# Kernel tuning notes

Hardware: AMD Instinct MI355X
Metric: run time of the kernel (lower is better)

The kernel has to match this reference:

```python
import jax, jax.numpy as jnp
import numpy as np

B, T, N_EMBED, HEAD = 512, 256, 384, 64
BLOCK = 256
SCALE = N_EMBED ** -0.5  # source scales by input-channel dim, not head_size


def setup_inputs() -> dict:
    key = jax.random.key(0)
    kx, kk, kq, kv = jax.random.split(key, 4)
    x = jax.random.normal(kx, (B, T, N_EMBED), dtype=jnp.float32)
    # torch Linear(n_embed, head_size, bias=False) weights, stored as (in, out)
    s = N_EMBED ** -0.5
    Wk = jax.random.normal(kk, (N_EMBED, HEAD), dtype=jnp.float32) * s
    Wq = jax.random.normal(kq, (N_EMBED, HEAD), dtype=jnp.float32) * s
    Wv = jax.random.normal(kv, (N_EMBED, HEAD), dtype=jnp.float32) * s
    return {"x": x, "Wk": Wk, "Wq": Wq, "Wv": Wv}


def reference(x, Wk, Wq, Wv):
    Bx, Tx, _ = x.shape
    K = jnp.einsum('btc,ch->bth', x, Wk)
    Q = jnp.einsum('btc,ch->bth', x, Wq)
    V = jnp.einsum('btc,ch->bth', x, Wv)
    scores = jnp.einsum('bth,bsh->bts', Q, K) * SCALE  # [B, T, T]
    causal = jnp.tril(jnp.ones((Tx, Tx), dtype=bool))
    scores = jnp.where(causal[None, :, :], scores, -jnp.inf)
    W = jax.nn.softmax(scores, axis=-1)
    # dropout is identity in eval mode (reference baseline is deterministic)
    out = jnp.einsum('bts,bsh->bth', W, V)
    return out
```

## Files before the change

kernel.cpp:

```cpp
#include <hip/hip_runtime.h>
#include <hip/hip_bf16.h>

#define B_  512
#define T_  256
#define C_  384
#define H_  64
#define SCALE_ 0.05103103630798287f

typedef float f32x4  __attribute__((ext_vector_type(4)));
typedef short bf16x8 __attribute__((ext_vector_type(8)));
typedef short bf16x4 __attribute__((ext_vector_type(4)));

__device__ __forceinline__ unsigned short f2bf(float f) {
    union { float f; unsigned u; } v; v.f = f;
    unsigned r = v.u + 0x7FFFu + ((v.u >> 16) & 1u);
    return (unsigned short)(r >> 16);
}
__device__ __forceinline__ unsigned cvt_pk_bf16(float lo, float hi) {
    unsigned r;
    asm("v_cvt_pk_bf16_f32 %0, %1, %2" : "=v"(r) : "v"(lo), "v"(hi));
    return r;
}
__device__ __forceinline__ int swz64(int row, int col) {
    return row * 64 + (((col >> 3) ^ (row & 7)) << 3) + (col & 7);
}

__global__ __launch_bounds__(1024, 4) void att_head_kernel(
    const float* __restrict__ x,  const float* __restrict__ Wk,
    const float* __restrict__ Wq, const float* __restrict__ Wv,
    float* __restrict__ out)
{
    __shared__ __align__(16) short smem[73728];
    short* const Ks = smem;
    short* const Vt = smem + 16384;
    short* const Pb = smem + 33280;

    const int tid  = threadIdx.x;
    const int b    = blockIdx.x;
    const int w    = tid >> 6;
    const int lane = tid & 63;
    const int g    = lane >> 4;
    const int i    = lane & 15;
    const int rb   = 16 * w;

    const float* xb = x + (size_t)b * T_ * C_;
    const float* Wm[3] = { Wk, Wq, Wv };

    f32x4 accP[12];
    #pragma unroll
    for (int nb = 0; nb < 12; nb++) accP[nb] = f32x4{0.f, 0.f, 0.f, 0.f};

    const float* xrow = xb + (size_t)(rb + i) * C_ + g * 8;

    {
        float wfa[12], wfb[12];
        auto loadWchunk = [&](int j, float* dst) {
            #pragma unroll
            for (int m = 0; m < 3; m++) {
                const float* Wp = Wm[m] + (size_t)(j * 64 + w * 4) * H_ + lane;
                #pragma unroll
                for (int jj = 0; jj < 4; jj++) dst[m * 4 + jj] = Wp[jj * H_];
            }
        };
        auto writeWchunk = [&](int j, const float* src) {
            short* buf = smem + j * 12288;
            #pragma unroll
            for (int m = 0; m < 3; m++) {
                union { unsigned u; short s[2]; } p0, p1;
                p0.u = cvt_pk_bf16(src[4 * m + 0], src[4 * m + 1]);
                p1.u = cvt_pk_bf16(src[4 * m + 2], src[4 * m + 3]);
                bf16x4 pk;
                pk[0] = p0.s[0]; pk[1] = p0.s[1]; pk[2] = p1.s[0]; pk[3] = p1.s[1];
                const int row = m * 64 + lane;
                const int k0  = w * 4;
                *(bf16x4*)&buf[row * 64 + (((k0 >> 3) ^ (row & 7)) << 3) + (k0 & 7)] = pk;
            }
        };
        loadWchunk(0, wfa);
        #pragma unroll
        for (int j = 0; j < 6; j++) {
            float* curW = (j & 1) ? wfb : wfa;
            float* nxtW = (j & 1) ? wfa : wfb;
            if (j < 5) loadWchunk(j + 1, nxtW);
            writeWchunk(j, curW);
        }
    }
    float4 xr[2][4];
    #pragma unroll
    for (int ks = 0; ks < 2; ks++)
        #pragma unroll
        for (int h = 0; h < 2; h++)
            xr[0][ks * 2 + h] = *(const float4*)(xrow + ks * 32 + h * 4);
    asm volatile("s_waitcnt lgkmcnt(0)\n\ts_barrier" ::: "memory");

    #pragma unroll
    for (int j = 0; j < 6; j++) {
        const int par = j & 1;
        const short* cur = smem + j * 12288;
        if (j < 5) {
            #pragma unroll
            for (int ks = 0; ks < 2; ks++)
                #pragma unroll
                for (int h = 0; h < 2; h++)
                    xr[par ^ 1][ks * 2 + h] = *(const float4*)(xrow + (j + 1) * 64 + ks * 32 + h * 4);
        }
        bf16x8 afs[2];
        #pragma unroll
        for (int ks = 0; ks < 2; ks++)
            #pragma unroll
            for (int h = 0; h < 2; h++) {
                const float4 v = xr[par][ks * 2 + h];
                afs[ks][h * 4 + 0] = (short)f2bf(v.x);
                afs[ks][h * 4 + 1] = (short)f2bf(v.y);
                afs[ks][h * 4 + 2] = (short)f2bf(v.z);
                afs[ks][h * 4 + 3] = (short)f2bf(v.w);
            }
        #pragma unroll
        for (int nb = 0; nb < 12; nb++) {
            #pragma unroll
            for (int ks = 0; ks < 2; ks++) {
                const int brow = nb * 16 + i;
                const bf16x8 bfr = *(const bf16x8*)&cur[brow * 64 + (((ks * 4 + g) ^ (i & 7)) << 3)];
                accP[nb] = __builtin_amdgcn_mfma_f32_16x16x32_bf16(afs[ks], bfr, accP[nb], 0, 0, 0);
            }
        }
    }
    asm volatile("s_waitcnt lgkmcnt(0)\n\ts_barrier" ::: "memory");

    #pragma unroll
    for (int nb = 0; nb < 4; nb++)
        #pragma unroll
        for (int r = 0; r < 4; r++)
            Ks[swz64(rb + 4 * g + r, 16 * nb + i)] = (short)f2bf(accP[4 + nb][r]);
    asm volatile("s_waitcnt lgkmcnt(0)" ::: "memory");
    bf16x8 qf[2];
    #pragma unroll
    for (int ks = 0; ks < 2; ks++)
        qf[ks] = *(const bf16x8*)&Ks[(rb + i) * 64 + (((4 * ks + g) ^ (i & 7)) << 3)];
    asm volatile("s_waitcnt lgkmcnt(0)" ::: "memory");
    #pragma unroll
    for (int nb = 0; nb < 4; nb++)
        #pragma unroll
        for (int r = 0; r < 4; r++)
            Ks[swz64(rb + 4 * g + r, 16 * nb + i)] = (short)f2bf(accP[nb][r]);
    #pragma unroll
    for (int nb = 0; nb < 4; nb++) {
        bf16x4 pk;
        #pragma unroll
        for (int r = 0; r < 4; r++) pk[r] = (short)f2bf(accP[8 + nb][r]);
        *(bf16x4*)&Vt[(16 * nb + i) * 264 + rb + 4 * g] = pk;
    }
    asm volatile("s_waitcnt lgkmcnt(0)\n\ts_barrier" ::: "memory");

    short* const myP = Pb + w * 1280;
    const float NEG_INF = -__builtin_inff();
    float mrun = NEG_INF, lrun = 0.f;
    f32x4 accO[4];
    #pragma unroll
    for (int ht = 0; ht < 4; ht++) accO[ht] = f32x4{0.f, 0.f, 0.f, 0.f};

    auto PVADD = [&](int bufsel, int ck) {
        const bf16x8 pf = *(const bf16x8*)&myP[bufsel * 640 + i * 40 + 8 * g];
        #pragma unroll
        for (int ht = 0; ht < 4; ht++) {
            const bf16x8 vf = *(const bf16x8*)&Vt[(16 * ht + i) * 264 + 32 * ck + 8 * g];
            accO[ht] = __builtin_amdgcn_mfma_f32_16x16x32_bf16(vf, pf, accO[ht], 0, 0, 0);
        }
    };

    const int npair = w >> 1;
    #pragma unroll
    for (int p = 0; p < 8; p++) {
        if (p <= npair) {
            f32x4 sA[2];
            sA[0] = f32x4{0.f, 0.f, 0.f, 0.f};
            sA[1] = f32x4{0.f, 0.f, 0.f, 0.f};
            #pragma unroll
            for (int s = 0; s < 2; s++) {
                const int nt = 2 * p + s;
                if (nt <= w) {
                    #pragma unroll
                    for (int ks = 0; ks < 2; ks++) {
                        const bf16x8 kfr = *(const bf16x8*)&Ks[(16 * nt + i) * 64 +
                                (((4 * ks + g) ^ (i & 7)) << 3)];
                        sA[s] = __builtin_amdgcn_mfma_f32_16x16x32_bf16(kfr, qf[ks], sA[s], 0, 0, 0);
                    }
                }
            }
            if (p > 0) PVADD((p - 1) & 1, p - 1);

            float mt = NEG_INF;
            #pragma unroll
            for (int s = 0; s < 2; s++)
                #pragma unroll
                for (int r = 0; r < 4; r++) {
                    const int kv = 16 * (2 * p + s) + 4 * g + r;
                    const bool ok = (2 * p + s <= w) && (kv <= rb + i);
                    const float v = ok ? sA[s][r] * SCALE_ : NEG_INF;
                    sA[s][r] = v;
                    mt = fmaxf(mt, v);
                }
            mt = fmaxf(mt, __shfl_xor(mt, 16, 64));
            mt = fmaxf(mt, __shfl_xor(mt, 32, 64));

            if (!__all(mt <= mrun + 8.0f)) {
                const float mnew = fmaxf(mrun, mt);
                const float f = __expf(mrun - mnew);
                mrun = mnew; lrun *= f;
                #pragma unroll
                for (int ht = 0; ht < 4; ht++)
                    #pragma unroll
                    for (int r = 0; r < 4; r++) accO[ht][r] *= f;
            }
            #pragma unroll
            for (int s = 0; s < 2; s++) {
                const float p0 = __expf(sA[s][0] - mrun);
                const float p1 = __expf(sA[s][1] - mrun);
                const float p2 = __expf(sA[s][2] - mrun);
                const float p3 = __expf(sA[s][3] - mrun);
                lrun += (p0 + p1) + (p2 + p3);
                union { bf16x4 v; unsigned u[2]; } pk;
                pk.u[0] = cvt_pk_bf16(p0, p1);
                pk.u[1] = cvt_pk_bf16(p2, p3);
                *(bf16x4*)&myP[(p & 1) * 640 + i * 40 + 16 * s + 4 * g] = pk.v;
            }
        }
    }
    PVADD(npair & 1, npair);

    lrun += __shfl_xor(lrun, 16, 64);
    lrun += __shfl_xor(lrun, 32, 64);
    const float inv = 1.f / lrun;

    float* orow = out + ((size_t)b * T_ + rb + i) * H_;
    #pragma unroll
    for (int ht = 0; ht < 4; ht++) {
        float4 o;
        o.x = accO[ht][0] * inv;
        o.y = accO[ht][1] * inv;
        o.z = accO[ht][2] * inv;
        o.w = accO[ht][3] * inv;
        *(float4*)&orow[16 * ht + 4 * g] = o;
    }
}

extern "C" void kernel_launch(void* const* d_in, const int* in_sizes, int n_in,
                              void* d_out, int out_size, void* d_ws, size_t ws_size,
                              hipStream_t stream) {
    const float* x  = (const float*)d_in[0];
    const float* Wk = (const float*)d_in[1];
    const float* Wq = (const float*)d_in[2];
    const float* Wv = (const float*)d_in[3];
    float* out = (float*)d_out;
    (void)d_ws; (void)ws_size; (void)in_sizes; (void)n_in; (void)out_size;
    att_head_kernel<<<dim3(B_), dim3(1024), 0, stream>>>(x, Wk, Wq, Wv, out);
}
```

Measured before the change: 56.89 us.

## Pre-transpose Wv to bf16 in workspace and read V weights from global

Adds a small pre-kernel that converts Wv to bf16 in a transposed layout inside the workspace. The main kernel then stages only Wk and Wq in shared memory and loads V-projection B fragments straight from global/L2. This shrinks LDS use per block and the per-block W staging work. The cost is an extra kernel launch and uncoalesced-ish global fragment loads inside the MFMA loop. The original kernel is kept as a fallback when no workspace is available.

```diff
diff --git a/kernel.cpp b/kernel.cpp
--- a/kernel.cpp
+++ b/kernel.cpp
@@ -25,12 +25,21 @@
     return row * 64 + (((col >> 3) ^ (row & 7)) << 3) + (col & 7);
 }
 
-__global__ __launch_bounds__(1024, 4) void att_head_kernel(
+__global__ void transpose_wv_kernel(const float* __restrict__ Wv, short* __restrict__ Wtv) {
+    const int idx = blockIdx.x * 256 + threadIdx.x;
+    const int n  = idx / 48;
+    const int kb = (idx % 48) * 8;
+    short* dst = Wtv + n * 384;
+    #pragma unroll
+    for (int k = kb; k < kb + 8; k++) dst[k] = (short)f2bf(Wv[(size_t)k * H_ + n]);
+}
+
+__global__ __launch_bounds__(1024, 4) void att_head_ws(
     const float* __restrict__ x,  const float* __restrict__ Wk,
-    const float* __restrict__ Wq, const float* __restrict__ Wv,
+    const float* __restrict__ Wq, const short* __restrict__ Wtv,
     float* __restrict__ out)
 {
-    __shared__ __align__(16) short smem[73728];
+    __shared__ __align__(16) short smem[53760];
     short* const Ks = smem;
     short* const Vt = smem + 16384;
     short* const Pb = smem + 33280;
@@ -44,7 +53,7 @@
     const int rb   = 16 * w;
 
     const float* xb = x + (size_t)b * T_ * C_;
-    const float* Wm[3] = { Wk, Wq, Wv };
+    const float* Wm[2] = { Wk, Wq };
 
     f32x4 accP[12];
     #pragma unroll
@@ -53,19 +62,19 @@
     const float* xrow = xb + (size_t)(rb + i) * C_ + g * 8;
 
     {
-        float wfa[12], wfb[12];
+        float wfa[8], wfb[8];
         auto loadWchunk = [&](int j, float* dst) {
             #pragma unroll
-            for (int m = 0; m < 3; m++) {
+            for (int m = 0; m < 2; m++) {
                 const float* Wp = Wm[m] + (size_t)(j * 64 + w * 4) * H_ + lane;
                 #pragma unroll
                 for (int jj = 0; jj < 4; jj++) dst[m * 4 + jj] = Wp[jj * H_];
             }
         };
         auto writeWchunk = [&](int j, const float* src) {
-            short* buf = smem + j * 12288;
-            #pragma unroll
-            for (int m = 0; m < 3; m++) {
+            short* buf = smem + j * 8192;
+            #pragma unroll
+            for (int m = 0; m < 2; m++) {
                 union { unsigned u; short s[2]; } p0, p1;
                 p0.u = cvt_pk_bf16(src[4 * m + 0], src[4 * m + 1]);
                 p1.u = cvt_pk_bf16(src[4 * m + 2], src[4 * m + 3]);
@@ -93,10 +102,11 @@
             xr[0][ks * 2 + h] = *(const float4*)(xrow + ks * 32 + h * 4);
     asm volatile("s_waitcnt lgkmcnt(0)\n\ts_barrier" ::: "memory");
 
+    const short* wtv0 = Wtv + (size_t)i * 384 + 8 * g;
     #pragma unroll
     for (int j = 0; j < 6; j++) {
         const int par = j & 1;
-        const short* cur = smem + j * 12288;
+        const short* cur = smem + j * 8192;
         if (j < 5) {
             #pragma unroll
             for (int ks = 0; ks < 2; ks++)
@@ -116,13 +126,20 @@
                 afs[ks][h * 4 + 3] = (short)f2bf(v.w);
             }
         #pragma unroll
-        for (int nb = 0; nb < 12; nb++) {
-            #pragma unroll
-            for (int ks = 0; ks < 2; ks++) {
+        for (int ks = 0; ks < 2; ks++) {
+            bf16x8 vf[4];
+            #pragma unroll
+            for (int nbv = 0; nbv < 4; nbv++)
+                vf[nbv] = *(const bf16x8*)(wtv0 + (size_t)(16 * nbv) * 384 + 64 * j + 32 * ks);
+            #pragma unroll
+            for (int nb = 0; nb < 8; nb++) {
                 const int brow = nb * 16 + i;
                 const bf16x8 bfr = *(const bf16x8*)&cur[brow * 64 + (((ks * 4 + g) ^ (i & 7)) << 3)];
                 accP[nb] = __builtin_amdgcn_mfma_f32_16x16x32_bf16(afs[ks], bfr, accP[nb], 0, 0, 0);
             }
+            #pragma unroll
+            for (int nbv = 0; nbv < 4; nbv++)
+                accP[8 + nbv] = __builtin_amdgcn_mfma_f32_16x16x32_bf16(afs[ks], vf[nbv], accP[8 + nbv], 0, 0, 0);
         }
     }
     asm volatile("s_waitcnt lgkmcnt(0)\n\ts_barrier" ::: "memory");
@@ -163,8 +180,8 @@
         const bf16x8 pf = *(const bf16x8*)&myP[bufsel * 640 + i * 40 + 8 * g];
         #pragma unroll
         for (int ht = 0; ht < 4; ht++) {
-            const bf16x8 vf = *(const bf16x8*)&Vt[(16 * ht + i) * 264 + 32 * ck + 8 * g];
-            accO[ht] = __builtin_amdgcn_mfma_f32_16x16x32_bf16(vf, pf, accO[ht], 0, 0, 0);
+            const bf16x8 vfx = *(const bf16x8*)&Vt[(16 * ht + i) * 264 + 32 * ck + 8 * g];
+            accO[ht] = __builtin_amdgcn_mfma_f32_16x16x32_bf16(vfx, pf, accO[ht], 0, 0, 0);
         }
     };
 
@@ -244,6 +261,225 @@
     }
 }
 
+__global__ __launch_bounds__(1024, 4) void att_head_kernel(
+    const float* __restrict__ x,  const float* __restrict__ Wk,
+    const float* __restrict__ Wq, const float* __restrict__ Wv,
+    float* __restrict__ out)
+{
+    __shared__ __align__(16) short smem[73728];
+    short* const Ks = smem;
+    short* const Vt = smem + 16384;
+    short* const Pb = smem + 33280;
+
+    const int tid  = threadIdx.x;
+    const int b    = blockIdx.x;
+    const int w    = tid >> 6;
+    const int lane = tid & 63;
+    const int g    = lane >> 4;
+    const int i    = lane & 15;
+    const int rb   = 16 * w;
+
+    const float* xb = x + (size_t)b * T_ * C_;
+    const float* Wm[3] = { Wk, Wq, Wv };
+
+    f32x4 accP[12];
+    #pragma unroll
+    for (int nb = 0; nb < 12; nb++) accP[nb] = f32x4{0.f, 0.f, 0.f, 0.f};
+
+    const float* xrow = xb + (size_t)(rb + i) * C_ + g * 8;
+
+    {
+        float wfa[12], wfb[12];
+        auto loadWchunk = [&](int j, float* dst) {
+            #pragma unroll
+            for (int m = 0; m < 3; m++) {
+                const float* Wp = Wm[m] + (size_t)(j * 64 + w * 4) * H_ + lane;
+                #pragma unroll
+                for (int jj = 0; jj < 4; jj++) dst[m * 4 + jj] = Wp[jj * H_];
+            }
+        };
+        auto writeWchunk = [&](int j, const float* src) {
+            short* buf = smem + j * 12288;
+            #pragma unroll
+            for (int m = 0; m < 3; m++) {
+                union { unsigned u; short s[2]; } p0, p1;
+                p0.u = cvt_pk_bf16(src[4 * m + 0], src[4 * m + 1]);
+                p1.u = cvt_pk_bf16(src[4 * m + 2], src[4 * m + 3]);
+                bf16x4 pk;
+                pk[0] = p0.s[0]; pk[1] = p0.s[1]; pk[2] = p1.s[0]; pk[3] = p1.s[1];
+                const int row = m * 64 + lane;
+                const int k0  = w * 4;
+                *(bf16x4*)&buf[row * 64 + (((k0 >> 3) ^ (row & 7)) << 3) + (k0 & 7)] = pk;
+            }
+        };
+        loadWchunk(0, wfa);
+        #pragma unroll
+        for (int j = 0; j < 6; j++) {
+            float* curW = (j & 1) ? wfb : wfa;
+            float* nxtW = (j & 1) ? wfa : wfb;
+            if (j < 5) loadWchunk(j + 1, nxtW);
+            writeWchunk(j, curW);
+        }
+    }
+    float4 xr[2][4];
+    #pragma unroll
+    for (int ks = 0; ks < 2; ks++)
+        #pragma unroll
+        for (int h = 0; h < 2; h++)
+            xr[0][ks * 2 + h] = *(const float4*)(xrow + ks * 32 + h * 4);
+    asm volatile("s_waitcnt lgkmcnt(0)\n\ts_barrier" ::: "memory");
+
+    #pragma unroll
+    for (int j = 0; j < 6; j++) {
+        const int par = j & 1;
+        const short* cur = smem + j * 12288;
+        if (j < 5) {
+            #pragma unroll
+            for (int ks = 0; ks < 2; ks++)
+                #pragma unroll
+                for (int h = 0; h < 2; h++)
+                    xr[par ^ 1][ks * 2 + h] = *(const float4*)(xrow + (j + 1) * 64 + ks * 32 + h * 4);
+        }
+        bf16x8 afs[2];
+        #pragma unroll
+        for (int ks = 0; ks < 2; ks++)
+            #pragma unroll
+            for (int h = 0; h < 2; h++) {
+                const float4 v = xr[par][ks * 2 + h];
+                afs[ks][h * 4 + 0] = (short)f2bf(v.x);
+                afs[ks][h * 4 + 1] = (short)f2bf(v.y);
+                afs[ks][h * 4 + 2] = (short)f2bf(v.z);
+                afs[ks][h * 4 + 3] = (short)f2bf(v.w);
+            }
+        #pragma unroll
+        for (int nb = 0; nb < 12; nb++) {
+            #pragma unroll
+            for (int ks = 0; ks < 2; ks++) {
+                const int brow = nb * 16 + i;
+                const bf16x8 bfr = *(const bf16x8*)&cur[brow * 64 + (((ks * 4 + g) ^ (i & 7)) << 3)];
+                accP[nb] = __builtin_amdgcn_mfma_f32_16x16x32_bf16(afs[ks], bfr, accP[nb], 0, 0, 0);
+            }
+        }
+    }
+    asm volatile("s_waitcnt lgkmcnt(0)\n\ts_barrier" ::: "memory");
+
+    #pragma unroll
+    for (int nb = 0; nb < 4; nb++)
+        #pragma unroll
+        for (int r = 0; r < 4; r++)
+            Ks[swz64(rb + 4 * g + r, 16 * nb + i)] = (short)f2bf(accP[4 + nb][r]);
+    asm volatile("s_waitcnt lgkmcnt(0)" ::: "memory");
+    bf16x8 qf[2];
+    #pragma unroll
+    for (int ks = 0; ks < 2; ks++)
+        qf[ks] = *(const bf16x8*)&Ks[(rb + i) * 64 + (((4 * ks + g) ^ (i & 7)) << 3)];
+    asm volatile("s_waitcnt lgkmcnt(0)" ::: "memory");
+    #pragma unroll
+    for (int nb = 0; nb < 4; nb++)
+        #pragma unroll
+        for (int r = 0; r < 4; r++)
+            Ks[swz64(rb + 4 * g + r, 16 * nb + i)] = (short)f2bf(accP[nb][r]);
+    #pragma unroll
+    for (int nb = 0; nb < 4; nb++) {
+        bf16x4 pk;
+        #pragma unroll
+        for (int r = 0; r < 4; r++) pk[r] = (short)f2bf(accP[8 + nb][r]);
+        *(bf16x4*)&Vt[(16 * nb + i) * 264 + rb + 4 * g] = pk;
+    }
+    asm volatile("s_waitcnt lgkmcnt(0)\n\ts_barrier" ::: "memory");
+
+    short* const myP = Pb + w * 1280;
+    const float NEG_INF = -__builtin_inff();
+    float mrun = NEG_INF, lrun = 0.f;
+    f32x4 accO[4];
+    #pragma unroll
+    for (int ht = 0; ht < 4; ht++) accO[ht] = f32x4{0.f, 0.f, 0.f, 0.f};
+
+    auto PVADD = [&](int bufsel, int ck) {
+        const bf16x8 pf = *(const bf16x8*)&myP[bufsel * 640 + i * 40 + 8 * g];
+        #pragma unroll
+        for (int ht = 0; ht < 4; ht++) {
+            const bf16x8 vfx = *(const bf16x8*)&Vt[(16 * ht + i) * 264 + 32 * ck + 8 * g];
+            accO[ht] = __builtin_amdgcn_mfma_f32_16x16x32_bf16(vfx, pf, accO[ht], 0, 0, 0);
+        }
+    };
+
+    const int npair = w >> 1;
+    #pragma unroll
+    for (int p = 0; p < 8; p++) {
+        if (p <= npair) {
+            f32x4 sA[2];
+            sA[0] = f32x4{0.f, 0.f, 0.f, 0.f};
+            sA[1] = f32x4{0.f, 0.f, 0.f, 0.f};
+            #pragma unroll
+            for (int s = 0; s < 2; s++) {
+                const int nt = 2 * p + s;
+                if (nt <= w) {
+                    #pragma unroll
+                    for (int ks = 0; ks < 2; ks++) {
+                        const bf16x8 kfr = *(const bf16x8*)&Ks[(16 * nt + i) * 64 +
+                                (((4 * ks + g) ^ (i & 7)) << 3)];
+                        sA[s] = __builtin_amdgcn_mfma_f32_16x16x32_bf16(kfr, qf[ks], sA[s], 0, 0, 0);
+                    }
+                }
+            }
+            if (p > 0) PVADD((p - 1) & 1, p - 1);
+
+            float mt = NEG_INF;
+            #pragma unroll
+            for (int s = 0; s < 2; s++)
+                #pragma unroll
+                for (int r = 0; r < 4; r++) {
+                    const int kv = 16 * (2 * p + s) + 4 * g + r;
+                    const bool ok = (2 * p + s <= w) && (kv <= rb + i);
+                    const float v = ok ? sA[s][r] * SCALE_ : NEG_INF;
+                    sA[s][r] = v;
+                    mt = fmaxf(mt, v);
+                }
+            mt = fmaxf(mt, __shfl_xor(mt, 16, 64));
+            mt = fmaxf(mt, __shfl_xor(mt, 32, 64));
+
+            if (!__all(mt <= mrun + 8.0f)) {
+                const float mnew = fmaxf(mrun, mt);
+                const float f = __expf(mrun - mnew);
+                mrun = mnew; lrun *= f;
+                #pragma unroll
+                for (int ht = 0; ht < 4; ht++)
+                    #pragma unroll
+                    for (int r = 0; r < 4; r++) accO[ht][r] *= f;
+            }
+            #pragma unroll
+            for (int s = 0; s < 2; s++) {
+                const float p0 = __expf(sA[s][0] - mrun);
+                const float p1 = __expf(sA[s][1] - mrun);
+                const float p2 = __expf(sA[s][2] - mrun);
+                const float p3 = __expf(sA[s][3] - mrun);
+                lrun += (p0 + p1) + (p2 + p3);
+                union { bf16x4 v; unsigned u[2]; } pk;
+                pk.u[0] = cvt_pk_bf16(p0, p1);
+                pk.u[1] = cvt_pk_bf16(p2, p3);
+                *(bf16x4*)&myP[(p & 1) * 640 + i * 40 + 16 * s + 4 * g] = pk.v;
+            }
+        }
+    }
+    PVADD(npair & 1, npair);
+
+    lrun += __shfl_xor(lrun, 16, 64);
+    lrun += __shfl_xor(lrun, 32, 64);
+    const float inv = 1.f / lrun;
+
+    float* orow = out + ((size_t)b * T_ + rb + i) * H_;
+    #pragma unroll
+    for (int ht = 0; ht < 4; ht++) {
+        float4 o;
+        o.x = accO[ht][0] * inv;
+        o.y = accO[ht][1] * inv;
+        o.z = accO[ht][2] * inv;
+        o.w = accO[ht][3] * inv;
+        *(float4*)&orow[16 * ht + 4 * g] = o;
+    }
+}
+
 extern "C" void kernel_launch(void* const* d_in, const int* in_sizes, int n_in,
                               void* d_out, int out_size, void* d_ws, size_t ws_size,
                               hipStream_t stream) {
@@ -252,6 +488,12 @@
     const float* Wq = (const float*)d_in[2];
     const float* Wv = (const float*)d_in[3];
     float* out = (float*)d_out;
-    (void)d_ws; (void)ws_size; (void)in_sizes; (void)n_in; (void)out_size;
-    att_head_kernel<<<dim3(B_), dim3(1024), 0, stream>>>(x, Wk, Wq, Wv, out);
-}
+    (void)in_sizes; (void)n_in; (void)out_size;
+    if (ws_size >= (size_t)(H_ * C_ * 2) && d_ws != nullptr) {
+        short* Wtv = (short*)d_ws;
+        transpose_wv_kernel<<<dim3(12), dim3(256), 0, stream>>>(Wv, Wtv);
+        att_head_ws<<<dim3(B_), dim3(1024), 0, stream>>>(x, Wk, Wq, Wtv, out);
+    } else {
+        att_head_kernel<<<dim3(B_), dim3(1024), 0, stream>>>(x, Wk, Wq, Wv, out);
+    }
+}
```

Result: slower. 93.45 us (+64.3%).
